# Kernel tuning notes

Measured on AMD Instinct MI355X. Metric: run time of the kernel, lower is better.

## Reference

```python
import jax, jax.numpy as jnp
import numpy as np

N_INSTR = 16384   # total instructions across all blocks
T_TOK   = 16      # max tokens per instruction
N_BLOCKS = 512    # number of basic blocks (batch)
MAX_BLK = 64      # max instructions per block
H = 128           # hidden_size
N_TOKENS = 1024   # vocab
P_INSTR = 32      # instr_param_size
P_GLOB = 8        # global_param_size
D_WORD = 2 * H + P_INSTR + P_GLOB  # word-LSTM input dim (bi char hidden + params)


def setup_inputs() -> dict:
    key = jax.random.key(0)
    ks = jax.random.split(key, 16)
    rng = np.random.default_rng(0)

    # ragged block lengths summing exactly to N_INSTR, values in [8, 56]
    bl = np.full(N_BLOCKS, N_INSTR // N_BLOCKS, dtype=np.int64)  # avg 32
    half = N_BLOCKS // 2
    delta = rng.integers(-24, 25, size=half)
    bl[:half] += delta
    bl[half:] -= delta
    block_lens = jnp.asarray(bl, dtype=jnp.int32)

    token_lens = jnp.asarray(rng.integers(4, T_TOK + 1, size=N_INSTR), dtype=jnp.int32)
    tokens = jax.random.randint(ks[0], (N_INSTR, T_TOK), 0, N_TOKENS, dtype=jnp.int32)

    instr_params = jax.random.normal(ks[1], (N_INSTR, P_INSTR), dtype=jnp.float32)
    global_params = jax.random.normal(ks[2], (N_BLOCKS, P_GLOB), dtype=jnp.float32)

    s = 1.0 / np.sqrt(H)
    def u(k, shape):
        return jax.random.uniform(k, shape, jnp.float32, -s, s)

    emb = jax.random.normal(ks[3], (N_TOKENS, H), dtype=jnp.float32) * 0.02
    # char LSTM (input dim H), forward and backward directions; b = b_ih + b_hh
    char_Wih_f = u(ks[4], (4 * H, H)); char_Whh_f = u(ks[5], (4 * H, H)); char_b_f = u(ks[6], (4 * H,))
    char_Wih_b = u(ks[7], (4 * H, H)); char_Whh_b = u(ks[8], (4 * H, H)); char_b_b = u(ks[9], (4 * H,))
    # word LSTM (input dim D_WORD)
    word_Wih_f = u(ks[10], (4 * H, D_WORD)); word_Whh_f = u(ks[11], (4 * H, H)); word_b_f = u(ks[12], (4 * H,))
    word_Wih_b = u(ks[13], (4 * H, D_WORD)); word_Whh_b = u(ks[14], (4 * H, H)); word_b_b = u(ks[15], (4 * H,))
    kf = jax.random.fold_in(key, 123)
    final_W = u(kf, (1, 2 * H + P_GLOB)); final_b = jnp.zeros((1,), jnp.float32)

    return dict(tokens=tokens, token_lens=token_lens, block_lens=block_lens,
                instr_params=instr_params, global_params=global_params, emb=emb,
                char_Wih_f=char_Wih_f, char_Whh_f=char_Whh_f, char_b_f=char_b_f,
                char_Wih_b=char_Wih_b, char_Whh_b=char_Whh_b, char_b_b=char_b_b,
                word_Wih_f=word_Wih_f, word_Whh_f=word_Whh_f, word_b_f=word_b_f,
                word_Wih_b=word_Wih_b, word_Whh_b=word_Whh_b, word_b_b=word_b_b,
                final_W=final_W, final_b=final_b)


def _run_dir(x, mask, Wih, Whh, b):
    # x: (B, T, D), mask: (B, T) bool. Masked LSTM scan; returns final hidden (B, H).
    B = x.shape[0]
    Hh = Whh.shape[1]
    def step(carry, inp):
        h, c = carry
        xt, m = inp                      # (B, D), (B,)
        g = xt @ Wih.T + h @ Whh.T + b   # (B, 4H)
        i, f, gg, o = jnp.split(g, 4, axis=-1)  # torch gate order i,f,g,o
        i = jax.nn.sigmoid(i); f = jax.nn.sigmoid(f)
        gg = jnp.tanh(gg); o = jax.nn.sigmoid(o)
        cn = f * c + i * gg
        hn = o * jnp.tanh(cn)
        m = m[:, None]
        return (jnp.where(m, hn, h), jnp.where(m, cn, c)), None
    init = (jnp.zeros((B, Hh), x.dtype), jnp.zeros((B, Hh), x.dtype))
    (h, _), _ = jax.lax.scan(step, init, (jnp.swapaxes(x, 0, 1), mask.T))
    return h


def _bilstm_final(x, lens, Wih_f, Whh_f, b_f, Wih_b, Whh_b, b_b):
    # final hidden of a 1-layer bi-LSTM over ragged sequences (pack_padded semantics)
    T = x.shape[1]
    t_idx = jnp.arange(T)
    mask = t_idx[None, :] < lens[:, None]          # (B, T)
    h_f = _run_dir(x, mask, Wih_f, Whh_f, b_f)
    rev_idx = jnp.maximum(lens[:, None] - 1 - t_idx[None, :], 0)  # valid prefix reversed
    x_rev = jnp.take_along_axis(x, rev_idx[:, :, None], axis=1)
    h_b = _run_dir(x_rev, mask, Wih_b, Whh_b, b_b)
    return jnp.concatenate([h_f, h_b], axis=-1)    # (B, 2H)


def reference(tokens, token_lens, block_lens, instr_params, global_params, emb,
              char_Wih_f, char_Whh_f, char_b_f, char_Wih_b, char_Whh_b, char_b_b,
              word_Wih_f, word_Whh_f, word_b_f, word_Wih_b, word_Whh_b, word_b_b,
              final_W, final_b):
    n_instr = tokens.shape[0]
    # char level: per-instruction bi-LSTM over token embeddings
    x = emb[tokens]                                # (N, T_TOK, H)
    instr_h = _bilstm_final(x, token_lens, char_Wih_f, char_Whh_f, char_b_f,
                            char_Wih_b, char_Whh_b, char_b_b)      # (N, 2H)
    instrs = jnp.concatenate([instr_h, instr_params], axis=1)      # (N, 2H+P_INSTR)
    # ragged re-pack: assign each instruction to its block and position
    ends = jnp.cumsum(block_lens)
    starts = ends - block_lens
    ar = jnp.arange(n_instr)
    bid = jnp.searchsorted(ends, ar, side='right')                 # block id per instr
    pos = ar - starts[bid]                                         # position within block
    full = jnp.concatenate([instrs, global_params[bid]], axis=1)   # (N, D_WORD)
    padded = jnp.zeros((block_lens.shape[0], MAX_BLK, full.shape[1]), full.dtype)
    padded = padded.at[bid, pos].set(full)                         # (B, MAX_BLK, D_WORD)
    # word level: per-block bi-LSTM over instruction summaries
    blocks_h = _bilstm_final(padded, block_lens, word_Wih_f, word_Whh_f, word_b_f,
                             word_Wih_b, word_Whh_b, word_b_b)     # (B, 2H)
    final_in = jnp.concatenate([blocks_h, global_params], axis=1)  # (B, 2H+P_GLOB)
    return final_in @ final_W.T + final_b                          # (B, 1)
```

## Files before the change

### kernel.cpp

```cpp
#include <hip/hip_runtime.h>
#include <hip/hip_bf16.h>
#include <math.h>

#define N_INSTR   16384
#define T_TOK     16
#define N_BLOCKS  512
#define MAX_BLK   64
#define HDIM      128
#define P_INSTR   32
#define P_GLOB    8
#define D_WORD    296
#define N_TOKENS  1024

#define CIB       16

__device__ __forceinline__ float sigf(float x) {
    return 1.0f / (1.0f + __expf(-x));
}
__device__ __forceinline__ float tanhf_s(float x) {
    float a = fabsf(x);
    float e = __expf(-2.0f * a);
    float t = (1.0f - e) / (1.0f + e);
    return copysignf(t, x);
}

__global__ __launch_bounds__(256) void prep_pack(
    const float* __restrict__ cWihF, const float* __restrict__ cWhhF,
    const float* __restrict__ cWihB, const float* __restrict__ cWhhB,
    const float* __restrict__ wWihF, const float* __restrict__ wWihB,
    const float* __restrict__ wWhhF, const float* __restrict__ wWhhB,
    float* __restrict__ W4cf, float* __restrict__ W4cb,
    float* __restrict__ W4p,  float* __restrict__ W4h)
{
    int idx = blockIdx.x * 256 + threadIdx.x;
    if (idx < 131072) {
        int kk = idx & 3, f = idx >> 2;
        int j = f & 511, k = ((f >> 9) << 2) + kk;
        W4cf[idx] = (k < 128) ? cWihF[j*128 + k] : cWhhF[j*128 + (k-128)];
    } else if (idx < 262144) {
        int id = idx - 131072;
        int kk = id & 3, f = id >> 2;
        int j = f & 511, k = ((f >> 9) << 2) + kk;
        W4cb[id] = (k < 128) ? cWihB[j*128 + k] : cWhhB[j*128 + (k-128)];
    } else if (idx < 262144 + 303104) {
        int id = idx - 262144;
        int kk = id & 3, f = id >> 2;
        int j = f & 1023, k = ((f >> 10) << 2) + kk;
        W4p[id] = (j < 512) ? wWihF[j*296 + k] : wWihB[(j-512)*296 + k];
    } else if (idx < 565248 + 131072) {
        int id = idx - 565248;
        int kk = id & 3, f = id >> 2;
        int j = f & 1023, k = ((f >> 10) << 2) + kk;
        W4h[id] = (j < 512) ? wWhhF[j*128 + k] : wWhhB[(j-512)*128 + k];
    }
}

__global__ __launch_bounds__(512) void scan_kernel(
    const int* __restrict__ block_lens, int* __restrict__ starts, int* __restrict__ bid)
{
    __shared__ int s[N_BLOCKS];
    int t = threadIdx.x;
    int len = block_lens[t];
    s[t] = len;
    __syncthreads();
    for (int off = 1; off < N_BLOCKS; off <<= 1) {
        int v = (t >= off) ? s[t - off] : 0;
        __syncthreads();
        s[t] += v;
        __syncthreads();
    }
    int start = s[t] - len;
    starts[t] = start;
    for (int p = 0; p < len; ++p) bid[start + p] = t;
}

__global__ __launch_bounds__(256) void sort_by_len(
    const int* __restrict__ token_lens, int* __restrict__ order)
{
    __shared__ int cnt[T_TOK + 1];
    __shared__ int base[T_TOK + 1];
    int tid = threadIdx.x;
    if (tid <= T_TOK) cnt[tid] = 0;
    __syncthreads();
    for (int i = tid; i < N_INSTR; i += 256) atomicAdd(&cnt[token_lens[i]], 1);
    __syncthreads();
    if (tid == 0) {
        int s = 0;
        for (int l = 0; l <= T_TOK; ++l) { base[l] = s; s += cnt[l]; }
    }
    __syncthreads();
    for (int i = tid; i < N_INSTR; i += 256) {
        int pos = atomicAdd(&base[token_lens[i]], 1);
        order[pos] = i;
    }
}

__global__ __launch_bounds__(512) void sort_blocks(
    const int* __restrict__ block_lens, int* __restrict__ border)
{
    __shared__ int cnt[MAX_BLK + 1];
    __shared__ int base[MAX_BLK + 1];
    int tid = threadIdx.x;
    if (tid <= MAX_BLK) cnt[tid] = 0;
    __syncthreads();
    int len = block_lens[tid];
    atomicAdd(&cnt[len], 1);
    __syncthreads();
    if (tid == 0) {
        int s = 0;
        for (int l = 0; l <= MAX_BLK; ++l) { base[l] = s; s += cnt[l]; }
    }
    __syncthreads();
    int pos = atomicAdd(&base[len], 1);
    border[pos] = tid;
}

__global__ __launch_bounds__(256) void ex_pack(
    const float* __restrict__ emb,
    const float* __restrict__ W4cf, const float* __restrict__ W4cb,
    float* __restrict__ EF4, float* __restrict__ EB4)
{
    __shared__ float xe[128];
    int tk  = blockIdx.x;
    int tid = threadIdx.x;
    if (tid < 32) ((float4*)xe)[tid] = ((const float4*)(emb + tk * HDIM))[tid];
    __syncthreads();
    int u = tid & 127, dir = tid >> 7;
    const float4* W = (const float4*)(dir ? W4cb : W4cf);
    float a0 = 0.f, a1 = 0.f, a2 = 0.f, a3 = 0.f;
    for (int kc = 0; kc < 32; ++kc) {
        float4 x  = ((const float4*)xe)[kc];
        float4 w0 = W[kc*512 +   0 + u];
        float4 w1 = W[kc*512 + 128 + u];
        float4 w2 = W[kc*512 + 256 + u];
        float4 w3 = W[kc*512 + 384 + u];
        a0 = fmaf(w0.x,x.x,fmaf(w0.y,x.y,fmaf(w0.z,x.z,fmaf(w0.w,x.w,a0))));
        a1 = fmaf(w1.x,x.x,fmaf(w1.y,x.y,fmaf(w1.z,x.z,fmaf(w1.w,x.w,a1))));
        a2 = fmaf(w2.x,x.x,fmaf(w2.y,x.y,fmaf(w2.z,x.z,fmaf(w2.w,x.w,a2))));
        a3 = fmaf(w3.x,x.x,fmaf(w3.y,x.y,fmaf(w3.z,x.z,fmaf(w3.w,x.w,a3))));
    }
    float4 r = make_float4(a0, a1, a2, a3);
    ((float4*)(dir ? EB4 : EF4))[tk * 128 + u] = r;
}

__global__ __launch_bounds__(256, 2) void char_lstm(
    const int* __restrict__ tokens, const int* __restrict__ token_lens,
    const int* __restrict__ order,
    const float* __restrict__ EF4, const float* __restrict__ EB4,
    const float* __restrict__ W4f, const float* __restrict__ W4b,
    const float* __restrict__ bf,  const float* __restrict__ bb,
    float* __restrict__ instr_h)
{
    __shared__ float hF[CIB][128];
    __shared__ float hB[CIB][128];
    __shared__ int   toks[CIB][T_TOK];
    __shared__ int   lens[CIB];
    __shared__ int   iid[CIB];
    __shared__ int   maxl_s;

    const int tid = threadIdx.x;
    const int i0  = blockIdx.x * CIB;

    if (tid == 0) maxl_s = 0;
    __syncthreads();
    if (tid < CIB) {
        int id = order[i0 + tid];
        iid[tid] = id;
        int l = token_lens[id];
        lens[tid] = l;
        atomicMax(&maxl_s, l);
    }
    __syncthreads();
    for (int idx = tid; idx < CIB * T_TOK; idx += 256)
        toks[idx >> 4][idx & 15] = tokens[iid[idx >> 4] * T_TOK + (idx & 15)];
    for (int idx = tid; idx < CIB * 128; idx += 256) {
        ((float*)hF)[idx] = 0.f;
        ((float*)hB)[idx] = 0.f;
    }
    __syncthreads();

    const int u    = tid & 127;
    const int half = tid >> 7;
    const int ib0  = half * 8;

    float bfr[4], bbr[4];
    #pragma unroll
    for (int g = 0; g < 4; ++g) { bfr[g] = bf[g*128 + u]; bbr[g] = bb[g*128 + u]; }

    float cF[8], cB[8];
    #pragma unroll
    for (int i = 0; i < 8; ++i) { cF[i] = 0.f; cB[i] = 0.f; }

    const float4* Wf = (const float4*)W4f + 32*512;
    const float4* Wb = (const float4*)W4b + 32*512;
    const float4* EF = (const float4*)EF4;
    const float4* EB = (const float4*)EB4;

    const int maxl = maxl_s;

    for (int t = 0; t < maxl; ++t) {
        {
            float acc[8][4];
            #pragma unroll
            for (int il = 0; il < 8; ++il) {
                float4 e = EF[toks[ib0 + il][t] * 128 + u];
                acc[il][0] = e.x; acc[il][1] = e.y; acc[il][2] = e.z; acc[il][3] = e.w;
            }
            for (int kc = 0; kc < 32; ++kc) {
                float4 w0 = Wf[kc*512 +   0 + u];
                float4 w1 = Wf[kc*512 + 128 + u];
                float4 w2 = Wf[kc*512 + 256 + u];
                float4 w3 = Wf[kc*512 + 384 + u];
                #pragma unroll
                for (int il = 0; il < 8; ++il) {
                    float4 x = *(const float4*)&hF[ib0 + il][kc*4];
                    acc[il][0] = fmaf(w0.x,x.x,fmaf(w0.y,x.y,fmaf(w0.z,x.z,fmaf(w0.w,x.w,acc[il][0]))));
                    acc[il][1] = fmaf(w1.x,x.x,fmaf(w1.y,x.y,fmaf(w1.z,x.z,fmaf(w1.w,x.w,acc[il][1]))));
                    acc[il][2] = fmaf(w2.x,x.x,fmaf(w2.y,x.y,fmaf(w2.z,x.z,fmaf(w2.w,x.w,acc[il][2]))));
                    acc[il][3] = fmaf(w3.x,x.x,fmaf(w3.y,x.y,fmaf(w3.z,x.z,fmaf(w3.w,x.w,acc[il][3]))));
                }
            }
            __syncthreads();
            #pragma unroll
            for (int il = 0; il < 8; ++il) {
                int i = ib0 + il;
                if (t < lens[i]) {
                    float gi = sigf   (acc[il][0] + bfr[0]);
                    float gf = sigf   (acc[il][1] + bfr[1]);
                    float gg = tanhf_s(acc[il][2] + bfr[2]);
                    float go = sigf   (acc[il][3] + bfr[3]);
                    float cn = gf * cF[il] + gi * gg;
                    cF[il] = cn;
                    hF[i][u] = go * tanhf_s(cn);
                }
            }
        }
        {
            float acc[8][4];
            #pragma unroll
            for (int il = 0; il < 8; ++il) {
                int i = ib0 + il;
                int tt = lens[i] - 1 - t;
                tt = tt < 0 ? 0 : tt;
                float4 e = EB[toks[i][tt] * 128 + u];
                acc[il][0] = e.x; acc[il][1] = e.y; acc[il][2] = e.z; acc[il][3] = e.w;
            }
            for (int kc = 0; kc < 32; ++kc) {
                float4 w0 = Wb[kc*512 +   0 + u];
                float4 w1 = Wb[kc*512 + 128 + u];
                float4 w2 = Wb[kc*512 + 256 + u];
                float4 w3 = Wb[kc*512 + 384 + u];
                #pragma unroll
                for (int il = 0; il < 8; ++il) {
                    float4 x = *(const float4*)&hB[ib0 + il][kc*4];
                    acc[il][0] = fmaf(w0.x,x.x,fmaf(w0.y,x.y,fmaf(w0.z,x.z,fmaf(w0.w,x.w,acc[il][0]))));
                    acc[il][1] = fmaf(w1.x,x.x,fmaf(w1.y,x.y,fmaf(w1.z,x.z,fmaf(w1.w,x.w,acc[il][1]))));
                    acc[il][2] = fmaf(w2.x,x.x,fmaf(w2.y,x.y,fmaf(w2.z,x.z,fmaf(w2.w,x.w,acc[il][2]))));
                    acc[il][3] = fmaf(w3.x,x.x,fmaf(w3.y,x.y,fmaf(w3.z,x.z,fmaf(w3.w,x.w,acc[il][3]))));
                }
            }
            __syncthreads();
            #pragma unroll
            for (int il = 0; il < 8; ++il) {
                int i = ib0 + il;
                if (t < lens[i]) {
                    float gi = sigf   (acc[il][0] + bbr[0]);
                    float gf = sigf   (acc[il][1] + bbr[1]);
                    float gg = tanhf_s(acc[il][2] + bbr[2]);
                    float go = sigf   (acc[il][3] + bbr[3]);
                    float cn = gf * cB[il] + gi * gg;
                    cB[il] = cn;
                    hB[i][u] = go * tanhf_s(cn);
                }
            }
        }
        __syncthreads();
    }

    for (int idx = tid; idx < CIB * 128; idx += 256) {
        int i = idx >> 7, uu = idx & 127;
        int id = iid[i];
        instr_h[id * 256 +       uu] = hF[i][uu];
        instr_h[id * 256 + 128 + uu] = hB[i][uu];
    }
}

__global__ __launch_bounds__(256) void xw_gather(
    const float* __restrict__ instr_h, const float* __restrict__ instr_params,
    const float* __restrict__ gparams, const int* __restrict__ bid,
    float* __restrict__ xw)
{
    int idx = blockIdx.x * 256 + threadIdx.x;
    if (idx >= N_INSTR * 74) return;
    int i = idx / 74, c = idx % 74;
    float4 v;
    if (c < 64)      v = ((const float4*)(instr_h + i*256))[c];
    else if (c < 72) v = ((const float4*)(instr_params + i*32))[c - 64];
    else             v = ((const float4*)(gparams + bid[i]*8))[c - 72];
    ((float4*)(xw + i*296))[c] = v;
}

__global__ __launch_bounds__(256) void word_proj(
    const float* __restrict__ xw, const float* __restrict__ W4p,
    const float* __restrict__ b_f, const float* __restrict__ b_b,
    float* __restrict__ P)
{
    __shared__ float xs[16][296];
    int tid = threadIdx.x;
    int rowTile = blockIdx.x >> 2;
    int colTile = blockIdx.x & 3;
    int i0 = rowTile * 16;

    for (int idx = tid; idx < 16 * 74; idx += 256) {
        int i = idx / 74, c = idx % 74;
        ((float4*)&xs[i][0])[c] = ((const float4*)(xw + (size_t)(i0 + i) * 296))[c];
    }
    __syncthreads();

    int j = colTile * 256 + tid;
    float acc[16];
    #pragma unroll
    for (int i = 0; i < 16; ++i) acc[i] = 0.f;
    const float4* W4 = (const float4*)W4p;
    for (int kc = 0; kc < 74; ++kc) {
        float4 w = W4[kc*1024 + j];
        #pragma unroll
        for (int i = 0; i < 16; ++i) {
            float4 x = ((const float4*)&xs[i][0])[kc];
            acc[i] = fmaf(w.x,x.x,fmaf(w.y,x.y,fmaf(w.z,x.z,fmaf(w.w,x.w,acc[i]))));
        }
    }
    float bias = (j < 512) ? b_f[j] : b_b[j - 512];
    for (int i = 0; i < 16; ++i)
        P[(size_t)(i0 + i) * 1024 + j] = acc[i] + bias;
}

__global__ __launch_bounds__(256, 2) void word_lstm(
    const float* __restrict__ W4h, const float* __restrict__ P,
    const int* __restrict__ starts, const int* __restrict__ block_lens,
    const int* __restrict__ border,
    float* __restrict__ hfin)
{
    __shared__ float hs[4][128];
    __shared__ int   binfo[4][3];

    const int w   = blockIdx.x;
    const int d   = w & 1;
    const int g   = w >> 1;
    const int tid = threadIdx.x;
    const int u    = tid & 127;
    const int half = tid >> 7;
    const int q0   = half * 2;

    if (tid < 4) {
        int ob = border[g * 4 + tid];
        binfo[tid][0] = ob;
        binfo[tid][1] = starts[ob];
        binfo[tid][2] = block_lens[ob];
    }
    for (int idx = tid; idx < 4 * 128; idx += 256) ((float*)hs)[idx] = 0.f;
    __syncthreads();

    const int len0 = binfo[q0][2],     len1 = binfo[q0 + 1][2];
    const int st0  = binfo[q0][1],     st1  = binfo[q0 + 1][1];
    const int maxlen = max(max(binfo[0][2], binfo[1][2]),
                           max(binfo[2][2], binfo[3][2]));

    float c0 = 0.f, c1 = 0.f;
    const float4* W4 = (const float4*)W4h;

    for (int t = 0; t < maxlen; ++t) {
        float a0[4] = {0.f, 0.f, 0.f, 0.f};
        float a1[4] = {0.f, 0.f, 0.f, 0.f};
        for (int kc = 0; kc < 32; ++kc) {
            float4 w0 = W4[kc*1024 + d*512 +   0 + u];
            float4 w1 = W4[kc*1024 + d*512 + 128 + u];
            float4 w2 = W4[kc*1024 + d*512 + 256 + u];
            float4 w3 = W4[kc*1024 + d*512 + 384 + u];
            float4 h0 = *(const float4*)&hs[q0][kc*4];
            float4 h1 = *(const float4*)&hs[q0 + 1][kc*4];
            a0[0] = fmaf(w0.x,h0.x,fmaf(w0.y,h0.y,fmaf(w0.z,h0.z,fmaf(w0.w,h0.w,a0[0]))));
            a0[1] = fmaf(w1.x,h0.x,fmaf(w1.y,h0.y,fmaf(w1.z,h0.z,fmaf(w1.w,h0.w,a0[1]))));
            a0[2] = fmaf(w2.x,h0.x,fmaf(w2.y,h0.y,fmaf(w2.z,h0.z,fmaf(w2.w,h0.w,a0[2]))));
            a0[3] = fmaf(w3.x,h0.x,fmaf(w3.y,h0.y,fmaf(w3.z,h0.z,fmaf(w3.w,h0.w,a0[3]))));
            a1[0] = fmaf(w0.x,h1.x,fmaf(w0.y,h1.y,fmaf(w0.z,h1.z,fmaf(w0.w,h1.w,a1[0]))));
            a1[1] = fmaf(w1.x,h1.x,fmaf(w1.y,h1.y,fmaf(w1.z,h1.z,fmaf(w1.w,h1.w,a1[1]))));
            a1[2] = fmaf(w2.x,h1.x,fmaf(w2.y,h1.y,fmaf(w2.z,h1.z,fmaf(w2.w,h1.w,a1[2]))));
            a1[3] = fmaf(w3.x,h1.x,fmaf(w3.y,h1.y,fmaf(w3.z,h1.z,fmaf(w3.w,h1.w,a1[3]))));
        }
        __syncthreads();
        if (t < len0) {
            int rs = (d == 0) ? (st0 + t) : (st0 + len0 - 1 - t);
            const float* Prow = P + (size_t)rs * 1024 + d * 512;
            float gi = sigf   (a0[0] + Prow[  0 + u]);
            float gf = sigf   (a0[1] + Prow[128 + u]);
            float gg = tanhf_s(a0[2] + Prow[256 + u]);
            float go = sigf   (a0[3] + Prow[384 + u]);
            float cn = gf * c0 + gi * gg;
            c0 = cn;
            hs[q0][u] = go * tanhf_s(cn);
        }
        if (t < len1) {
            int rs = (d == 0) ? (st1 + t) : (st1 + len1 - 1 - t);
            const float* Prow = P + (size_t)rs * 1024 + d * 512;
            float gi = sigf   (a1[0] + Prow[  0 + u]);
            float gf = sigf   (a1[1] + Prow[128 + u]);
            float gg = tanhf_s(a1[2] + Prow[256 + u]);
            float go = sigf   (a1[3] + Prow[384 + u]);
            float cn = gf * c1 + gi * gg;
            c1 = cn;
            hs[q0 + 1][u] = go * tanhf_s(cn);
        }
        __syncthreads();
    }

    hfin[(size_t)(d * 512 + binfo[q0][0])     * 128 + u] = hs[q0][u];
    hfin[(size_t)(d * 512 + binfo[q0 + 1][0]) * 128 + u] = hs[q0 + 1][u];
}

__global__ __launch_bounds__(256) void final_k(
    const float* __restrict__ hfinal, const float* __restrict__ gp,
    const float* __restrict__ fW, const float* __restrict__ fb,
    float* __restrict__ out)
{
    int tid = threadIdx.x;
    int w = tid >> 6, l = tid & 63;
    int b = blockIdx.x * 4 + w;
    const float* hf = hfinal + (size_t)(0 * 512 + b) * 128;
    const float* hb = hfinal + (size_t)(1 * 512 + b) * 128;
    float s = hf[l] * fW[l] + hf[l + 64] * fW[l + 64]
            + hb[l] * fW[128 + l] + hb[l + 64] * fW[192 + l];
    if (l < 8) s += gp[b * 8 + l] * fW[256 + l];
    #pragma unroll
    for (int off = 32; off > 0; off >>= 1) s += __shfl_down(s, off);
    if (l == 0) out[b] = s + fb[0];
}

extern "C" void kernel_launch(void* const* d_in, const int* in_sizes, int n_in,
                              void* d_out, int out_size, void* d_ws, size_t ws_size,
                              hipStream_t stream)
{
    const int*   tokens        = (const int*)  d_in[0];
    const int*   token_lens    = (const int*)  d_in[1];
    const int*   block_lens    = (const int*)  d_in[2];
    const float* instr_params  = (const float*)d_in[3];
    const float* global_params = (const float*)d_in[4];
    const float* emb           = (const float*)d_in[5];
    const float* cWihF = (const float*)d_in[6];
    const float* cWhhF = (const float*)d_in[7];
    const float* cbF   = (const float*)d_in[8];
    const float* cWihB = (const float*)d_in[9];
    const float* cWhhB = (const float*)d_in[10];
    const float* cbB   = (const float*)d_in[11];
    const float* wWihF = (const float*)d_in[12];
    const float* wWhhF = (const float*)d_in[13];
    const float* wbF   = (const float*)d_in[14];
    const float* wWihB = (const float*)d_in[15];
    const float* wWhhB = (const float*)d_in[16];
    const float* wbB   = (const float*)d_in[17];
    const float* fW    = (const float*)d_in[18];
    const float* fb    = (const float*)d_in[19];
    float* out = (float*)d_out;

    char* ws = (char*)d_ws;
    size_t off = 0;
    auto alloc_f = [&](size_t nfloats) { float* p = (float*)(ws + off); off += nfloats * 4; return p; };

    float* W4cf    = alloc_f(131072);
    float* W4cb    = alloc_f(131072);
    float* W4p     = alloc_f(303104);
    float* W4h     = alloc_f(131072);
    float* instr_h = alloc_f((size_t)N_INSTR * 256);
    float* xw      = alloc_f((size_t)N_INSTR * 296);
    float* P       = alloc_f((size_t)N_INSTR * 1024);
    float* hfin    = alloc_f(2 * 512 * 128);
    float* EF4     = alloc_f((size_t)N_TOKENS * 128 * 4);
    float* EB4     = alloc_f((size_t)N_TOKENS * 128 * 4);
    int*   starts  = (int*)(ws + off); off += 512 * 4;
    int*   bid     = (int*)(ws + off); off += N_INSTR * 4;
    int*   order   = (int*)(ws + off); off += N_INSTR * 4;
    int*   border  = (int*)(ws + off); off += 512 * 4;

    prep_pack<<<2720, 256, 0, stream>>>(cWihF, cWhhF, cWihB, cWhhB,
                                        wWihF, wWihB, wWhhF, wWhhB,
                                        W4cf, W4cb, W4p, W4h);
    scan_kernel<<<1, 512, 0, stream>>>(block_lens, starts, bid);
    sort_by_len<<<1, 256, 0, stream>>>(token_lens, order);
    sort_blocks<<<1, 512, 0, stream>>>(block_lens, border);
    ex_pack<<<N_TOKENS, 256, 0, stream>>>(emb, W4cf, W4cb, EF4, EB4);

    char_lstm<<<N_INSTR / CIB, 256, 0, stream>>>(tokens, token_lens, order,
                                                 EF4, EB4, W4cf, W4cb,
                                                 cbF, cbB, instr_h);
    xw_gather<<<4736, 256, 0, stream>>>(instr_h, instr_params, global_params, bid, xw);
    word_proj<<<4096, 256, 0, stream>>>(xw, W4p, wbF, wbB, P);
    word_lstm<<<256, 256, 0, stream>>>(W4h, P, starts, block_lens, border, hfin);
    final_k<<<128, 256, 0, stream>>>(hfin, global_params, fW, fb, out);
}
```

Before: 1.431 ms.

## Run char-LSTM recurrent matmul on MFMA with split-bf16 precision

Moves the char-LSTM hidden-to-gate product off scalar FMA loops and onto bf16 MFMA instructions. Both the weights and the hidden state are split into hi and lo bf16 parts, and three MFMAs per tile keep near-fp32 accuracy. A new kernel pre-packs the recurrent weights into the MFMA B-fragment layout. The gate bias is folded into the embedding projection table, and each workgroup now handles 32 instructions instead of 16. This trades extra MFMA work and bf16 split/merge overhead for much higher matmul throughput, with a small accuracy risk from the three-term split.

Result: slower. 1.517 ms (+6.0%).

```diff
diff --git a/kernel.cpp b/kernel.cpp
--- a/kernel.cpp
+++ b/kernel.cpp
@@ -12,7 +12,11 @@
 #define D_WORD    296
 #define N_TOKENS  1024
 
-#define CIB       16
+#define CIB       32
+#define HPAD      136
+
+typedef short s16x8 __attribute__((ext_vector_type(8)));
+typedef float f32x4 __attribute__((ext_vector_type(4)));
 
 __device__ __forceinline__ float sigf(float x) {
     return 1.0f / (1.0f + __expf(-x));
@@ -22,6 +26,14 @@
     float e = __expf(-2.0f * a);
     float t = (1.0f - e) / (1.0f + e);
     return copysignf(t, x);
+}
+__device__ __forceinline__ ushort f2bf(float f) {
+    unsigned u = __float_as_uint(f);
+    unsigned r = u + 0x7FFFu + ((u >> 16) & 1u);
+    return (ushort)(r >> 16);
+}
+__device__ __forceinline__ float bf2f(ushort h) {
+    return __uint_as_float(((unsigned)h) << 16);
 }
 
 __global__ __launch_bounds__(256) void prep_pack(
@@ -55,6 +67,30 @@
     }
 }
 
+__global__ __launch_bounds__(256) void pack_bfrag(
+    const float* __restrict__ cWhhF, const float* __restrict__ cWhhB,
+    ushort* __restrict__ Bf)
+{
+    int F = blockIdx.x * 256 + threadIdx.x;
+    if (F >= 32768) return;
+    int lane = F & 63; int q = F >> 6;
+    int hl = q & 1; q >>= 1;
+    int j  = q & 7; q >>= 3;
+    int kk = q & 3; q >>= 2;
+    int w  = q & 3; q >>= 2;
+    int dir = q;
+    const float* W = dir ? cWhhB : cWhhF;
+    int n = w + 4 * j;
+    int gate = n * 16 + (lane & 15);
+    int k0 = kk * 32 + (lane >> 4) * 8;
+    #pragma unroll
+    for (int jj = 0; jj < 8; ++jj) {
+        float wv = W[gate * 128 + k0 + jj];
+        ushort h = f2bf(wv);
+        Bf[(size_t)F * 8 + jj] = hl ? f2bf(wv - bf2f(h)) : h;
+    }
+}
+
 __global__ __launch_bounds__(512) void scan_kernel(
     const int* __restrict__ block_lens, int* __restrict__ starts, int* __restrict__ bid)
 {
@@ -118,6 +154,7 @@
 __global__ __launch_bounds__(256) void ex_pack(
     const float* __restrict__ emb,
     const float* __restrict__ W4cf, const float* __restrict__ W4cb,
+    const float* __restrict__ cbF,  const float* __restrict__ cbB,
     float* __restrict__ EF4, float* __restrict__ EB4)
 {
     __shared__ float xe[128];
@@ -127,6 +164,7 @@
     __syncthreads();
     int u = tid & 127, dir = tid >> 7;
     const float4* W = (const float4*)(dir ? W4cb : W4cf);
+    const float*  B = dir ? cbB : cbF;
     float a0 = 0.f, a1 = 0.f, a2 = 0.f, a3 = 0.f;
     for (int kc = 0; kc < 32; ++kc) {
         float4 x  = ((const float4*)xe)[kc];
@@ -139,7 +177,7 @@
         a2 = fmaf(w2.x,x.x,fmaf(w2.y,x.y,fmaf(w2.z,x.z,fmaf(w2.w,x.w,a2))));
         a3 = fmaf(w3.x,x.x,fmaf(w3.y,x.y,fmaf(w3.z,x.z,fmaf(w3.w,x.w,a3))));
     }
-    float4 r = make_float4(a0, a1, a2, a3);
+    float4 r = make_float4(a0 + B[u], a1 + B[128+u], a2 + B[256+u], a3 + B[384+u]);
     ((float4*)(dir ? EB4 : EF4))[tk * 128 + u] = r;
 }
 
@@ -147,16 +185,15 @@
     const int* __restrict__ tokens, const int* __restrict__ token_lens,
     const int* __restrict__ order,
     const float* __restrict__ EF4, const float* __restrict__ EB4,
-    const float* __restrict__ W4f, const float* __restrict__ W4b,
-    const float* __restrict__ bf,  const float* __restrict__ bb,
+    const ushort* __restrict__ Bfrag,
     float* __restrict__ instr_h)
 {
-    __shared__ float hF[CIB][128];
-    __shared__ float hB[CIB][128];
-    __shared__ int   toks[CIB][T_TOK];
-    __shared__ int   lens[CIB];
-    __shared__ int   iid[CIB];
-    __shared__ int   maxl_s;
+    __shared__ ushort hhi[2][CIB][HPAD];
+    __shared__ ushort hlo[2][CIB][HPAD];
+    __shared__ int    toks_s[CIB][T_TOK];
+    __shared__ int    lens_s[CIB];
+    __shared__ int    iid[CIB];
+    __shared__ int    maxl_s;
 
     const int tid = threadIdx.x;
     const int i0  = blockIdx.x * CIB;
@@ -166,122 +203,118 @@
     if (tid < CIB) {
         int id = order[i0 + tid];
         iid[tid] = id;
-        int l = token_lens[id];
-        lens[tid] = l;
-        atomicMax(&maxl_s, l);
+        int ln = token_lens[id];
+        lens_s[tid] = ln;
+        atomicMax(&maxl_s, ln);
     }
     __syncthreads();
     for (int idx = tid; idx < CIB * T_TOK; idx += 256)
-        toks[idx >> 4][idx & 15] = tokens[iid[idx >> 4] * T_TOK + (idx & 15)];
-    for (int idx = tid; idx < CIB * 128; idx += 256) {
-        ((float*)hF)[idx] = 0.f;
-        ((float*)hB)[idx] = 0.f;
-    }
-    __syncthreads();
-
-    const int u    = tid & 127;
-    const int half = tid >> 7;
-    const int ib0  = half * 8;
-
-    float bfr[4], bbr[4];
+        toks_s[idx >> 4][idx & 15] = tokens[iid[idx >> 4] * T_TOK + (idx & 15)];
+    for (int idx = tid; idx < 2 * CIB * HPAD; idx += 256) {
+        ((ushort*)hhi)[idx] = 0;
+        ((ushort*)hlo)[idx] = 0;
+    }
+    __syncthreads();
+
+    const int l   = tid & 63;
+    const int w   = tid >> 6;
+    const int col = l & 15;
+    const int hi4 = l >> 4;
+    const int u0  = w * 16 + col;
+    const int u1  = (w + 4) * 16 + col;
+
+    int lenr[8];
     #pragma unroll
-    for (int g = 0; g < 4; ++g) { bfr[g] = bf[g*128 + u]; bbr[g] = bb[g*128 + u]; }
-
-    float cF[8], cB[8];
+    for (int m = 0; m < 2; ++m)
+        #pragma unroll
+        for (int reg = 0; reg < 4; ++reg)
+            lenr[m*4 + reg] = lens_s[m*16 + hi4*4 + reg];
+
+    float cst[2][16];
     #pragma unroll
-    for (int i = 0; i < 8; ++i) { cF[i] = 0.f; cB[i] = 0.f; }
-
-    const float4* Wf = (const float4*)W4f + 32*512;
-    const float4* Wb = (const float4*)W4b + 32*512;
-    const float4* EF = (const float4*)EF4;
-    const float4* EB = (const float4*)EB4;
-
+    for (int d = 0; d < 2; ++d)
+        #pragma unroll
+        for (int c = 0; c < 16; ++c) cst[d][c] = 0.f;
+
+    const s16x8* Bfv = (const s16x8*)Bfrag;
     const int maxl = maxl_s;
 
     for (int t = 0; t < maxl; ++t) {
-        {
-            float acc[8][4];
+        #pragma unroll
+        for (int dir = 0; dir < 2; ++dir) {
+            const float4* Ep = dir ? (const float4*)EB4 : (const float4*)EF4;
+            f32x4 acc[2][8];
             #pragma unroll
-            for (int il = 0; il < 8; ++il) {
-                float4 e = EF[toks[ib0 + il][t] * 128 + u];
-                acc[il][0] = e.x; acc[il][1] = e.y; acc[il][2] = e.z; acc[il][3] = e.w;
+            for (int m = 0; m < 2; ++m) {
+                #pragma unroll
+                for (int reg = 0; reg < 4; ++reg) {
+                    int i  = m*16 + hi4*4 + reg;
+                    int ln = lenr[m*4 + reg];
+                    int tt = dir ? (ln - 1 - t) : t;
+                    tt = tt < 0 ? 0 : tt;
+                    int tok = toks_s[i][tt];
+                    float4 e0 = Ep[tok * 128 + u0];
+                    float4 e1 = Ep[tok * 128 + u1];
+                    acc[m][0][reg] = e0.x; acc[m][2][reg] = e0.y;
+                    acc[m][4][reg] = e0.z; acc[m][6][reg] = e0.w;
+                    acc[m][1][reg] = e1.x; acc[m][3][reg] = e1.y;
+                    acc[m][5][reg] = e1.z; acc[m][7][reg] = e1.w;
+                }
             }
-            for (int kc = 0; kc < 32; ++kc) {
-                float4 w0 = Wf[kc*512 +   0 + u];
-                float4 w1 = Wf[kc*512 + 128 + u];
-                float4 w2 = Wf[kc*512 + 256 + u];
-                float4 w3 = Wf[kc*512 + 384 + u];
+            #pragma unroll
+            for (int kk = 0; kk < 4; ++kk) {
+                int cofs = kk*32 + hi4*8;
+                s16x8 a0h = *(const s16x8*)&hhi[dir][col     ][cofs];
+                s16x8 a0l = *(const s16x8*)&hlo[dir][col     ][cofs];
+                s16x8 a1h = *(const s16x8*)&hhi[dir][16 + col][cofs];
+                s16x8 a1l = *(const s16x8*)&hlo[dir][16 + col][cofs];
+                const s16x8* bp = Bfv + (size_t)(((dir*4 + w)*4 + kk)) * 1024;
                 #pragma unroll
-                for (int il = 0; il < 8; ++il) {
-                    float4 x = *(const float4*)&hF[ib0 + il][kc*4];
-                    acc[il][0] = fmaf(w0.x,x.x,fmaf(w0.y,x.y,fmaf(w0.z,x.z,fmaf(w0.w,x.w,acc[il][0]))));
-                    acc[il][1] = fmaf(w1.x,x.x,fmaf(w1.y,x.y,fmaf(w1.z,x.z,fmaf(w1.w,x.w,acc[il][1]))));
-                    acc[il][2] = fmaf(w2.x,x.x,fmaf(w2.y,x.y,fmaf(w2.z,x.z,fmaf(w2.w,x.w,acc[il][2]))));
-                    acc[il][3] = fmaf(w3.x,x.x,fmaf(w3.y,x.y,fmaf(w3.z,x.z,fmaf(w3.w,x.w,acc[il][3]))));
+                for (int j = 0; j < 8; ++j) {
+                    s16x8 bh = bp[(2*j + 0)*64 + l];
+                    s16x8 bl = bp[(2*j + 1)*64 + l];
+                    acc[0][j] = __builtin_amdgcn_mfma_f32_16x16x32_bf16(a0h, bh, acc[0][j], 0, 0, 0);
+                    acc[0][j] = __builtin_amdgcn_mfma_f32_16x16x32_bf16(a0l, bh, acc[0][j], 0, 0, 0);
+                    acc[0][j] = __builtin_amdgcn_mfma_f32_16x16x32_bf16(a0h, bl, acc[0][j], 0, 0, 0);
+                    acc[1][j] = __builtin_amdgcn_mfma_f32_16x16x32_bf16(a1h, bh, acc[1][j], 0, 0, 0);
+                    acc[1][j] = __builtin_amdgcn_mfma_f32_16x16x32_bf16(a1l, bh, acc[1][j], 0, 0, 0);
+                    acc[1][j] = __builtin_amdgcn_mfma_f32_16x16x32_bf16(a1h, bl, acc[1][j], 0, 0, 0);
                 }
             }
             __syncthreads();
             #pragma unroll
-            for (int il = 0; il < 8; ++il) {
-                int i = ib0 + il;
-                if (t < lens[i]) {
-                    float gi = sigf   (acc[il][0] + bfr[0]);
-                    float gf = sigf   (acc[il][1] + bfr[1]);
-                    float gg = tanhf_s(acc[il][2] + bfr[2]);
-                    float go = sigf   (acc[il][3] + bfr[3]);
-                    float cn = gf * cF[il] + gi * gg;
-                    cF[il] = cn;
-                    hF[i][u] = go * tanhf_s(cn);
-                }
-            }
-        }
-        {
-            float acc[8][4];
-            #pragma unroll
-            for (int il = 0; il < 8; ++il) {
-                int i = ib0 + il;
-                int tt = lens[i] - 1 - t;
-                tt = tt < 0 ? 0 : tt;
-                float4 e = EB[toks[i][tt] * 128 + u];
-                acc[il][0] = e.x; acc[il][1] = e.y; acc[il][2] = e.z; acc[il][3] = e.w;
-            }
-            for (int kc = 0; kc < 32; ++kc) {
-                float4 w0 = Wb[kc*512 +   0 + u];
-                float4 w1 = Wb[kc*512 + 128 + u];
-                float4 w2 = Wb[kc*512 + 256 + u];
-                float4 w3 = Wb[kc*512 + 384 + u];
+            for (int m = 0; m < 2; ++m) {
                 #pragma unroll
-                for (int il = 0; il < 8; ++il) {
-                    float4 x = *(const float4*)&hB[ib0 + il][kc*4];
-                    acc[il][0] = fmaf(w0.x,x.x,fmaf(w0.y,x.y,fmaf(w0.z,x.z,fmaf(w0.w,x.w,acc[il][0]))));
-                    acc[il][1] = fmaf(w1.x,x.x,fmaf(w1.y,x.y,fmaf(w1.z,x.z,fmaf(w1.w,x.w,acc[il][1]))));
-                    acc[il][2] = fmaf(w2.x,x.x,fmaf(w2.y,x.y,fmaf(w2.z,x.z,fmaf(w2.w,x.w,acc[il][2]))));
-                    acc[il][3] = fmaf(w3.x,x.x,fmaf(w3.y,x.y,fmaf(w3.z,x.z,fmaf(w3.w,x.w,acc[il][3]))));
+                for (int ug = 0; ug < 2; ++ug) {
+                    #pragma unroll
+                    for (int reg = 0; reg < 4; ++reg) {
+                        int i = m*16 + hi4*4 + reg;
+                        if (t < lenr[m*4 + reg]) {
+                            float gi = sigf   (acc[m][0 + ug][reg]);
+                            float gf = sigf   (acc[m][2 + ug][reg]);
+                            float gg = tanhf_s(acc[m][4 + ug][reg]);
+                            float go = sigf   (acc[m][6 + ug][reg]);
+                            int ci = m*8 + ug*4 + reg;
+                            float cn = gf * cst[dir][ci] + gi * gg;
+                            cst[dir][ci] = cn;
+                            float h = go * tanhf_s(cn);
+                            ushort hh = f2bf(h);
+                            int uu = ug ? u1 : u0;
+                            hhi[dir][i][uu] = hh;
+                            hlo[dir][i][uu] = f2bf(h - bf2f(hh));
+                        }
+                    }
                 }
             }
             __syncthreads();
-            #pragma unroll
-            for (int il = 0; il < 8; ++il) {
-                int i = ib0 + il;
-                if (t < lens[i]) {
-                    float gi = sigf   (acc[il][0] + bbr[0]);
-                    float gf = sigf   (acc[il][1] + bbr[1]);
-                    float gg = tanhf_s(acc[il][2] + bbr[2]);
-                    float go = sigf   (acc[il][3] + bbr[3]);
-                    float cn = gf * cB[il] + gi * gg;
-                    cB[il] = cn;
-                    hB[i][u] = go * tanhf_s(cn);
-                }
-            }
         }
-        __syncthreads();
     }
 
     for (int idx = tid; idx < CIB * 128; idx += 256) {
         int i = idx >> 7, uu = idx & 127;
         int id = iid[i];
-        instr_h[id * 256 +       uu] = hF[i][uu];
-        instr_h[id * 256 + 128 + uu] = hB[i][uu];
+        instr_h[id * 256 +       uu] = bf2f(hhi[0][i][uu]) + bf2f(hlo[0][i][uu]);
+        instr_h[id * 256 + 128 + uu] = bf2f(hhi[1][i][uu]) + bf2f(hlo[1][i][uu]);
     }
 }
 
@@ -470,6 +503,7 @@
     float* W4cb    = alloc_f(131072);
     float* W4p     = alloc_f(303104);
     float* W4h     = alloc_f(131072);
+    float* Bfrag   = alloc_f(131072);
     float* instr_h = alloc_f((size_t)N_INSTR * 256);
     float* xw      = alloc_f((size_t)N_INSTR * 296);
     float* P       = alloc_f((size_t)N_INSTR * 1024);
@@ -484,14 +518,15 @@
     prep_pack<<<2720, 256, 0, stream>>>(cWihF, cWhhF, cWihB, cWhhB,
                                         wWihF, wWihB, wWhhF, wWhhB,
                                         W4cf, W4cb, W4p, W4h);
+    pack_bfrag<<<128, 256, 0, stream>>>(cWhhF, cWhhB, (ushort*)Bfrag);
     scan_kernel<<<1, 512, 0, stream>>>(block_lens, starts, bid);
     sort_by_len<<<1, 256, 0, stream>>>(token_lens, order);
     sort_blocks<<<1, 512, 0, stream>>>(block_lens, border);
-    ex_pack<<<N_TOKENS, 256, 0, stream>>>(emb, W4cf, W4cb, EF4, EB4);
+    ex_pack<<<N_TOKENS, 256, 0, stream>>>(emb, W4cf, W4cb, cbF, cbB, EF4, EB4);
 
     char_lstm<<<N_INSTR / CIB, 256, 0, stream>>>(tokens, token_lens, order,
-                                                 EF4, EB4, W4cf, W4cb,
-                                                 cbF, cbB, instr_h);
+                                                 EF4, EB4, (const ushort*)Bfrag,
+                                                 instr_h);
     xw_gather<<<4736, 256, 0, stream>>>(instr_h, instr_params, global_params, bid, xw);
     word_proj<<<4096, 256, 0, stream>>>(xw, W4p, wbF, wbB, P);
     word_lstm<<<256, 256, 0, stream>>>(W4h, P, starts, block_lens, border, hfin);
```
